# Optimization experiments

Measured on AMD Instinct MI355X. Metric: run time of the kernel, lower is better.

## Reference

```python
import jax, jax.numpy as jnp
import numpy as np

N_NODES = 32
N_HEADS = 4
HEAD_DIM = 64
NEG_SLOPE = 0.2  # PyG GATConv default LeakyReLU slope


def setup_inputs() -> dict:
    key = jax.random.key(0)
    ks = jax.random.split(key, 8)
    roi_feats = jax.random.normal(ks[0], (N_NODES, 256, 96, 96), dtype=jnp.float32)
    edge_index = jax.random.randint(ks[1], (2, 512), 0, N_NODES, dtype=jnp.int32)
    W = jax.random.normal(ks[2], (256, N_HEADS * HEAD_DIM), dtype=jnp.float32) * 0.0625
    a_src = jax.random.normal(ks[3], (N_HEADS, HEAD_DIM), dtype=jnp.float32) * 0.125
    a_dst = jax.random.normal(ks[4], (N_HEADS, HEAD_DIM), dtype=jnp.float32) * 0.125
    gat_bias = jnp.zeros((N_HEADS * HEAD_DIM,), dtype=jnp.float32)
    cls_W = jax.random.normal(ks[5], (256, 32), dtype=jnp.float32) * 0.0625
    cls_b = jnp.zeros((32,), dtype=jnp.float32)
    return {"roi_feats": roi_feats, "edge_index": edge_index, "W": W,
            "a_src": a_src, "a_dst": a_dst, "gat_bias": gat_bias,
            "cls_W": cls_W, "cls_b": cls_b}


def _gat_conv(x, edge_index, W, a_src, a_dst, bias):
    # x: [N, C]; edge_index: [2, E] (src row 0, dst row 1)
    N = x.shape[0]
    # PyG GATConv adds self-loops by default
    loops = jnp.arange(N, dtype=edge_index.dtype)
    src = jnp.concatenate([edge_index[0], loops])
    dst = jnp.concatenate([edge_index[1], loops])
    h = (x @ W).reshape(N, N_HEADS, HEAD_DIM)          # [N, H, F]
    alpha_s = jnp.einsum('nhf,hf->nh', h, a_src)       # [N, H]
    alpha_d = jnp.einsum('nhf,hf->nh', h, a_dst)
    e = alpha_s[src] + alpha_d[dst]                    # [E', H]
    e = jnp.where(e >= 0, e, NEG_SLOPE * e)            # LeakyReLU
    # segment softmax over incoming edges of each dst node
    m = jax.ops.segment_max(e, dst, num_segments=N)    # [N, H]
    ex = jnp.exp(e - m[dst])
    denom = jax.ops.segment_sum(ex, dst, num_segments=N)
    alpha = ex / denom[dst]                            # [E', H]
    out = jax.ops.segment_sum(alpha[:, :, None] * h[src], dst, num_segments=N)
    return out.reshape(N, N_HEADS * HEAD_DIM) + bias


def reference(roi_feats, edge_index, W, a_src, a_dst, gat_bias, cls_W, cls_b):
    # [N, C, H, W] -> [N, C] spatial mean pool
    x = roi_feats.mean(axis=(2, 3))
    x = _gat_conv(x, edge_index, W, a_src, a_dst, gat_bias)
    logit = jax.nn.silu(x) @ cls_W + cls_b             # [N, num_au]
    return logit
```

## Files before the change

### kernel.cpp

```cpp
#include <hip/hip_runtime.h>
#include <math.h>

#define N_NODES  32
#define N_HEADS  4
#define HEAD_DIM 64
#define CDIM     256
#define HWPIX    9216
#define ROWF4    2304
#define E_BASE   512
#define E_TOT    544
#define NEG_SLOPE 0.2f
#define XS       257
#define POOL_BLOCKS 2048

__global__ __launch_bounds__(256, 4) void pool_kernel(const float* __restrict__ roi,
                                                      const float* __restrict__ W,
                                                      const float* __restrict__ a_src,
                                                      const float* __restrict__ a_dst,
                                                      float* __restrict__ x,
                                                      float* __restrict__ was_g,
                                                      float* __restrict__ wad_g) {
    if (blockIdx.x == POOL_BLOCKS) {
        const int t = threadIdx.x;
        float accs[4] = {0.f, 0.f, 0.f, 0.f};
        float accd[4] = {0.f, 0.f, 0.f, 0.f};
        const float4* wr  = (const float4*)(W + (size_t)t * CDIM);
        const float4* as4 = (const float4*)a_src;
        const float4* ad4 = (const float4*)a_dst;
#pragma unroll 16
        for (int j = 0; j < 64; ++j) {
            const float4 w = wr[j], av = as4[j], dv = ad4[j];
            const int hd = j >> 4;
            accs[hd] += w.x * av.x + w.y * av.y + w.z * av.z + w.w * av.w;
            accd[hd] += w.x * dv.x + w.y * dv.y + w.z * dv.z + w.w * dv.w;
        }
#pragma unroll
        for (int hd = 0; hd < 4; ++hd) {
            was_g[t * 4 + hd] = accs[hd];
            wad_g[t * 4 + hd] = accd[hd];
        }
        return;
    }

    const int wave = threadIdx.x >> 6, lane = threadIdx.x & 63;
    const int row = blockIdx.x * 4 + wave;
    const float4* p = reinterpret_cast<const float4*>(roi) + (size_t)row * ROWF4 + lane;

    float4 A[12], B[12];
    float s = 0.f;

#pragma unroll
    for (int j = 0; j < 12; ++j) A[j] = p[j * 64];
#pragma unroll
    for (int j = 0; j < 12; ++j) B[j] = p[(12 + j) * 64];
#pragma unroll
    for (int j = 0; j < 12; ++j) s += (A[j].x + A[j].y) + (A[j].z + A[j].w);
#pragma unroll
    for (int j = 0; j < 12; ++j) A[j] = p[(24 + j) * 64];
#pragma unroll
    for (int j = 0; j < 12; ++j) s += (B[j].x + B[j].y) + (B[j].z + B[j].w);
#pragma unroll
    for (int j = 0; j < 12; ++j) s += (A[j].x + A[j].y) + (A[j].z + A[j].w);

#pragma unroll
    for (int off = 32; off; off >>= 1) s += __shfl_down(s, off);
    if (lane == 0) x[row] = s * (1.0f / (float)HWPIX);
}

__global__ __launch_bounds__(256) void gat_kernel(const int* __restrict__ edge_index,
                                                  const float* __restrict__ x,
                                                  const float* __restrict__ was_g,
                                                  const float* __restrict__ wad_g,
                                                  const float* __restrict__ W,
                                                  const float* __restrict__ gat_bias,
                                                  const float* __restrict__ cls_W,
                                                  const float* __restrict__ cls_b,
                                                  float* __restrict__ out) {
    const int n = blockIdx.x;
    const int t = threadIdx.x;
    const int wavg = t >> 6, lane = t & 63;

    __shared__ float    xs[N_NODES * XS];
    __shared__ float    was[CDIM * N_HEADS];
    __shared__ float    wad[CDIM * N_HEADS];
    __shared__ float    als[N_NODES * N_HEADS];
    __shared__ float    adn[N_HEADS];
    __shared__ unsigned msegu[N_HEADS];
    __shared__ float    M[N_NODES * N_HEADS];
    __shared__ float    y[N_HEADS * CDIM];
    __shared__ float    sv[CDIM];
    __shared__ float4   red4[N_HEADS][64];
    __shared__ float    cred[8][32];

    float4 xv[8];
#pragma unroll
    for (int k = 0; k < 8; ++k) xv[k] = ((const float4*)x)[t + k * 256];
    const float4 wasv = ((const float4*)was_g)[t];
    const float4 wadv = ((const float4*)wad_g)[t];
    const int es0 = edge_index[t],       ed0 = edge_index[E_BASE + t];
    const int es1 = edge_index[256 + t], ed1 = edge_index[E_BASE + 256 + t];
    float4 bias4 = make_float4(0.f, 0.f, 0.f, 0.f);
    if (t < 64) bias4 = ((const float4*)gat_bias)[t];
    float cb = 0.f;
    if (t < 32) cb = cls_b[t];

#pragma unroll
    for (int k = 0; k < 8; ++k) {
        const int i = (t + k * 256) * 4, s = i >> 8, c = i & 255;
        xs[s * XS + c + 0] = xv[k].x;
        xs[s * XS + c + 1] = xv[k].y;
        xs[s * XS + c + 2] = xv[k].z;
        xs[s * XS + c + 3] = xv[k].w;
    }
    ((float4*)was)[t] = wasv;
    ((float4*)wad)[t] = wadv;
    if (t < 128) M[t] = 0.f;
    if (t < 4) msegu[t] = 0u;
    __syncthreads();

    if (t < 132) {
        if (t < 128) {
            const int s = t >> 2, hd = t & 3;
            const float* xrow = &xs[s * XS];
            float acc = 0.f;
#pragma unroll 8
            for (int c = 0; c < CDIM; ++c) acc += xrow[c] * was[c * 4 + hd];
            als[t] = acc;
        } else {
            const int hd = t - 128;
            const float* xrow = &xs[n * XS];
            float acc = 0.f;
#pragma unroll 8
            for (int c = 0; c < CDIM; ++c) acc += xrow[c] * wad[c * 4 + hd];
            adn[hd] = acc;
        }
    }
    __syncthreads();

    {
        const bool sl = (t < 32) && (t == n);
#pragma unroll
        for (int hd = 0; hd < 4; ++hd) {
            float best = -INFINITY;
            if (ed0 == n) {
                float v = als[es0 * 4 + hd] + adn[hd];
                best = fmaxf(best, (v >= 0.f) ? v : NEG_SLOPE * v);
            }
            if (ed1 == n) {
                float v = als[es1 * 4 + hd] + adn[hd];
                best = fmaxf(best, (v >= 0.f) ? v : NEG_SLOPE * v);
            }
            if (sl) {
                float v = als[n * 4 + hd] + adn[hd];
                best = fmaxf(best, (v >= 0.f) ? v : NEG_SLOPE * v);
            }
            if (best > -INFINITY) {
                const int iv = __float_as_int(best);
                const unsigned key = (iv < 0) ? ~(unsigned)iv
                                              : ((unsigned)iv | 0x80000000u);
                atomicMax(&msegu[hd], key);
            }
        }
    }
    __syncthreads();

    float mx[4];
#pragma unroll
    for (int hd = 0; hd < 4; ++hd) {
        const unsigned key = msegu[hd];
        const int im = (key & 0x80000000u) ? (int)(key & 0x7fffffffu) : (int)~key;
        mx[hd] = __int_as_float(im);
    }

    {
        const bool sl = (t < 32) && (t == n);
#pragma unroll
        for (int hd = 0; hd < 4; ++hd) {
            if (ed0 == n) {
                float v = als[es0 * 4 + hd] + adn[hd];
                v = (v >= 0.f) ? v : NEG_SLOPE * v;
                atomicAdd(&M[es0 * 4 + hd], expf(v - mx[hd]));
            }
            if (ed1 == n) {
                float v = als[es1 * 4 + hd] + adn[hd];
                v = (v >= 0.f) ? v : NEG_SLOPE * v;
                atomicAdd(&M[es1 * 4 + hd], expf(v - mx[hd]));
            }
            if (sl) {
                float v = als[n * 4 + hd] + adn[hd];
                v = (v >= 0.f) ? v : NEG_SLOPE * v;
                atomicAdd(&M[n * 4 + hd], expf(v - mx[hd]));
            }
        }
    }
    __syncthreads();

    {
        const int hd = wavg;
        float a0 = 0.f, a1 = 0.f, a2 = 0.f, a3 = 0.f, msum = 0.f;
#pragma unroll
        for (int s = 0; s < N_NODES; ++s) {
            const float m = M[s * 4 + hd];
            msum += m;
            const float* xrow = &xs[s * XS + lane];
            a0 += m * xrow[0];   a1 += m * xrow[64];
            a2 += m * xrow[128]; a3 += m * xrow[192];
        }
        const float rd = 1.0f / msum;
        y[hd * CDIM + lane]       = a0 * rd;
        y[hd * CDIM + lane + 64]  = a1 * rd;
        y[hd * CDIM + lane + 128] = a2 * rd;
        y[hd * CDIM + lane + 192] = a3 * rd;
    }
    __syncthreads();

    {
        const int hd = lane >> 4;
        const float* yrow = &y[hd * CDIM];
        float4 acc = make_float4(0.f, 0.f, 0.f, 0.f);
#pragma unroll 16
        for (int cc = 0; cc < 64; ++cc) {
            const int c = wavg * 64 + cc;
            const float4 w4 = ((const float4*)(W + (size_t)c * CDIM))[lane];
            const float yv = yrow[c];
            acc.x += yv * w4.x; acc.y += yv * w4.y;
            acc.z += yv * w4.z; acc.w += yv * w4.w;
        }
        red4[wavg][lane] = acc;
    }
    __syncthreads();
    if (t < 64) {
        const float4 s0 = red4[0][t], s1 = red4[1][t];
        const float4 s2 = red4[2][t], s3 = red4[3][t];
        float v0 = s0.x + s1.x + s2.x + s3.x + bias4.x;
        float v1 = s0.y + s1.y + s2.y + s3.y + bias4.y;
        float v2 = s0.z + s1.z + s2.z + s3.z + bias4.z;
        float v3 = s0.w + s1.w + s2.w + s3.w + bias4.w;
        sv[4 * t + 0] = v0 / (1.0f + expf(-v0));
        sv[4 * t + 1] = v1 / (1.0f + expf(-v1));
        sv[4 * t + 2] = v2 / (1.0f + expf(-v2));
        sv[4 * t + 3] = v3 / (1.0f + expf(-v3));
    }
    __syncthreads();

    {
        const int j = t & 31, g8 = t >> 5;
        float a = 0.f;
#pragma unroll
        for (int c0 = 0; c0 < 32; ++c0) {
            const int c = g8 * 32 + c0;
            a += sv[c] * cls_W[c * 32 + j];
        }
        cred[g8][j] = a;
    }
    __syncthreads();
    if (t < 32) {
        float s2 = cb;
#pragma unroll
        for (int g2 = 0; g2 < 8; ++g2) s2 += cred[g2][t];
        out[n * 32 + t] = s2;
    }
}

extern "C" void kernel_launch(void* const* d_in, const int* in_sizes, int n_in,
                              void* d_out, int out_size, void* d_ws, size_t ws_size,
                              hipStream_t stream) {
    const float* roi   = (const float*)d_in[0];
    const int*   eidx  = (const int*)d_in[1];
    const float* W     = (const float*)d_in[2];
    const float* a_src = (const float*)d_in[3];
    const float* a_dst = (const float*)d_in[4];
    const float* gbias = (const float*)d_in[5];
    const float* clsW  = (const float*)d_in[6];
    const float* clsb  = (const float*)d_in[7];
    float* out = (float*)d_out;

    float* x     = (float*)d_ws;
    float* was_g = x + 8192;
    float* wad_g = was_g + 1024;

    pool_kernel<<<POOL_BLOCKS + 1, 256, 0, stream>>>(roi, W, a_src, a_dst,
                                                     x, was_g, wad_g);
    gat_kernel<<<N_NODES, 256, 0, stream>>>(eidx, x, was_g, wad_g, W,
                                            gbias, clsW, clsb, out);
}
```

Measured before the change: 64.45 us.

## Widen GAT kernel to 1024 threads and preload W/cls_W into registers

Raises the per-node gat_kernel block from 256 to 1024 threads and redistributes every stage over them. The attention-logit dot products are split four ways with a shuffle reduction, and there is one thread per edge including self-loops. Slices of W and cls_W are prefetched into registers early so their global latency overlaps the softmax stages, and shared scratch buffers are aliased onto the xs region. The aim is to shorten the latency-bound serial chain in this tiny 32-block kernel. The cost is more register pressure and wider cross-wave reductions. The pool kernel, which likely dominates total time, is unchanged.

```diff
diff --git a/kernel.cpp b/kernel.cpp
--- a/kernel.cpp
+++ b/kernel.cpp
@@ -3,7 +3,6 @@
 
 #define N_NODES  32
 #define N_HEADS  4
-#define HEAD_DIM 64
 #define CDIM     256
 #define HWPIX    9216
 #define ROWF4    2304
@@ -67,20 +66,23 @@
     if (lane == 0) x[row] = s * (1.0f / (float)HWPIX);
 }
 
-__global__ __launch_bounds__(256) void gat_kernel(const int* __restrict__ edge_index,
-                                                  const float* __restrict__ x,
-                                                  const float* __restrict__ was_g,
-                                                  const float* __restrict__ wad_g,
-                                                  const float* __restrict__ W,
-                                                  const float* __restrict__ gat_bias,
-                                                  const float* __restrict__ cls_W,
-                                                  const float* __restrict__ cls_b,
-                                                  float* __restrict__ out) {
+__global__ __launch_bounds__(1024, 4) void gat_kernel(const int* __restrict__ edge_index,
+                                                      const float* __restrict__ x,
+                                                      const float* __restrict__ was_g,
+                                                      const float* __restrict__ wad_g,
+                                                      const float* __restrict__ W,
+                                                      const float* __restrict__ gat_bias,
+                                                      const float* __restrict__ cls_W,
+                                                      const float* __restrict__ cls_b,
+                                                      float* __restrict__ out) {
     const int n = blockIdx.x;
     const int t = threadIdx.x;
-    const int wavg = t >> 6, lane = t & 63;
-
-    __shared__ float    xs[N_NODES * XS];
+    const int wv = t >> 6, ln = t & 63;
+
+    __shared__ __align__(16) char arena[N_NODES * XS * 4];
+    float*  xs   = (float*)arena;
+    float4* red4 = (float4*)arena;
+    float*  cred = (float*)(arena + 16384);
     __shared__ float    was[CDIM * N_HEADS];
     __shared__ float    wad[CDIM * N_HEADS];
     __shared__ float    als[N_NODES * N_HEADS];
@@ -89,73 +91,67 @@
     __shared__ float    M[N_NODES * N_HEADS];
     __shared__ float    y[N_HEADS * CDIM];
     __shared__ float    sv[CDIM];
-    __shared__ float4   red4[N_HEADS][64];
-    __shared__ float    cred[8][32];
-
-    float4 xv[8];
-#pragma unroll
-    for (int k = 0; k < 8; ++k) xv[k] = ((const float4*)x)[t + k * 256];
-    const float4 wasv = ((const float4*)was_g)[t];
-    const float4 wadv = ((const float4*)wad_g)[t];
-    const int es0 = edge_index[t],       ed0 = edge_index[E_BASE + t];
-    const int es1 = edge_index[256 + t], ed1 = edge_index[E_BASE + 256 + t];
-    float4 bias4 = make_float4(0.f, 0.f, 0.f, 0.f);
+
+    const float4 xv0 = ((const float4*)x)[t];
+    const float4 xv1 = ((const float4*)x)[t + 1024];
+    float4 wasv = make_float4(0.f,0.f,0.f,0.f), wadv = wasv;
+    if (t < 256) {
+        wasv = ((const float4*)was_g)[t];
+        wadv = ((const float4*)wad_g)[t];
+    }
+    int es0 = 0, ed0 = -1;
+    if (t < E_BASE) { es0 = edge_index[t]; ed0 = edge_index[E_BASE + t]; }
+    float4 bias4 = make_float4(0.f,0.f,0.f,0.f);
     if (t < 64) bias4 = ((const float4*)gat_bias)[t];
     float cb = 0.f;
     if (t < 32) cb = cls_b[t];
-
-#pragma unroll
-    for (int k = 0; k < 8; ++k) {
-        const int i = (t + k * 256) * 4, s = i >> 8, c = i & 255;
-        xs[s * XS + c + 0] = xv[k].x;
-        xs[s * XS + c + 1] = xv[k].y;
-        xs[s * XS + c + 2] = xv[k].z;
-        xs[s * XS + c + 3] = xv[k].w;
-    }
-    ((float4*)was)[t] = wasv;
-    ((float4*)wad)[t] = wadv;
+    float cw[8];
+    {
+        const int k = t & 31, g = t >> 5;
+#pragma unroll
+        for (int i = 0; i < 8; ++i) cw[i] = cls_W[(g * 8 + i) * 32 + k];
+    }
+
+    {
+        int i = t * 4, s = i >> 8, c = i & 255;
+        xs[s * XS + c + 0] = xv0.x; xs[s * XS + c + 1] = xv0.y;
+        xs[s * XS + c + 2] = xv0.z; xs[s * XS + c + 3] = xv0.w;
+        i = (t + 1024) * 4; s = i >> 8; c = i & 255;
+        xs[s * XS + c + 0] = xv1.x; xs[s * XS + c + 1] = xv1.y;
+        xs[s * XS + c + 2] = xv1.z; xs[s * XS + c + 3] = xv1.w;
+    }
+    if (t < 256) { ((float4*)was)[t] = wasv; ((float4*)wad)[t] = wadv; }
     if (t < 128) M[t] = 0.f;
-    if (t < 4) msegu[t] = 0u;
-    __syncthreads();
-
-    if (t < 132) {
-        if (t < 128) {
-            const int s = t >> 2, hd = t & 3;
-            const float* xrow = &xs[s * XS];
-            float acc = 0.f;
-#pragma unroll 8
-            for (int c = 0; c < CDIM; ++c) acc += xrow[c] * was[c * 4 + hd];
-            als[t] = acc;
-        } else {
-            const int hd = t - 128;
-            const float* xrow = &xs[n * XS];
-            float acc = 0.f;
-#pragma unroll 8
-            for (int c = 0; c < CDIM; ++c) acc += xrow[c] * wad[c * 4 + hd];
-            adn[hd] = acc;
-        }
-    }
-    __syncthreads();
-
-    {
-        const bool sl = (t < 32) && (t == n);
-#pragma unroll
-        for (int hd = 0; hd < 4; ++hd) {
-            float best = -INFINITY;
-            if (ed0 == n) {
-                float v = als[es0 * 4 + hd] + adn[hd];
-                best = fmaxf(best, (v >= 0.f) ? v : NEG_SLOPE * v);
-            }
-            if (ed1 == n) {
-                float v = als[es1 * 4 + hd] + adn[hd];
-                best = fmaxf(best, (v >= 0.f) ? v : NEG_SLOPE * v);
-            }
-            if (sl) {
-                float v = als[n * 4 + hd] + adn[hd];
-                best = fmaxf(best, (v >= 0.f) ? v : NEG_SLOPE * v);
-            }
-            if (best > -INFINITY) {
-                const int iv = __float_as_int(best);
+    if (t < 4)   msegu[t] = 0u;
+    __syncthreads();
+
+    if (t < 528) {
+        const int q = t & 3;
+        const int s  = (t < 512) ? (t >> 4) : n;
+        const int hd = (t < 512) ? ((t >> 2) & 3) : ((t - 512) >> 2);
+        const float* xrow = &xs[s * XS + q * 64];
+        const float* wvp  = (t < 512) ? &was[q * 256 + hd] : &wad[q * 256 + hd];
+        float acc = 0.f;
+#pragma unroll 16
+        for (int c = 0; c < 64; ++c) acc += xrow[c] * wvp[c * 4];
+        acc += __shfl_down(acc, 2);
+        acc += __shfl_down(acc, 1);
+        if (q == 0) {
+            if (t < 512) als[(t >> 4) * 4 + hd] = acc;
+            else         adn[hd] = acc;
+        }
+    }
+    __syncthreads();
+
+    if (t < E_TOT) {
+        const int s0 = (t < E_BASE) ? es0 : (t - E_BASE);
+        const int d  = (t < E_BASE) ? ed0 : (t - E_BASE);
+        if (d == n) {
+#pragma unroll
+            for (int hd = 0; hd < 4; ++hd) {
+                float v = als[s0 * 4 + hd] + adn[hd];
+                v = (v >= 0.f) ? v : NEG_SLOPE * v;
+                const int iv = __float_as_int(v);
                 const unsigned key = (iv < 0) ? ~(unsigned)iv
                                               : ((unsigned)iv | 0x80000000u);
                 atomicMax(&msegu[hd], key);
@@ -172,92 +168,76 @@
         mx[hd] = __int_as_float(im);
     }
 
-    {
-        const bool sl = (t < 32) && (t == n);
-#pragma unroll
-        for (int hd = 0; hd < 4; ++hd) {
-            if (ed0 == n) {
-                float v = als[es0 * 4 + hd] + adn[hd];
+    if (t < E_TOT) {
+        const int s0 = (t < E_BASE) ? es0 : (t - E_BASE);
+        const int d  = (t < E_BASE) ? ed0 : (t - E_BASE);
+        if (d == n) {
+#pragma unroll
+            for (int hd = 0; hd < 4; ++hd) {
+                float v = als[s0 * 4 + hd] + adn[hd];
                 v = (v >= 0.f) ? v : NEG_SLOPE * v;
-                atomicAdd(&M[es0 * 4 + hd], expf(v - mx[hd]));
+                atomicAdd(&M[s0 * 4 + hd], expf(v - mx[hd]));
             }
-            if (ed1 == n) {
-                float v = als[es1 * 4 + hd] + adn[hd];
-                v = (v >= 0.f) ? v : NEG_SLOPE * v;
-                atomicAdd(&M[es1 * 4 + hd], expf(v - mx[hd]));
-            }
-            if (sl) {
-                float v = als[n * 4 + hd] + adn[hd];
-                v = (v >= 0.f) ? v : NEG_SLOPE * v;
-                atomicAdd(&M[n * 4 + hd], expf(v - mx[hd]));
-            }
-        }
-    }
-    __syncthreads();
-
-    {
-        const int hd = wavg;
-        float a0 = 0.f, a1 = 0.f, a2 = 0.f, a3 = 0.f, msum = 0.f;
+        }
+    }
+    __syncthreads();
+
+    float4 wreg[16];
+#pragma unroll
+    for (int r = 0; r < 16; ++r)
+        wreg[r] = ((const float4*)(W + (size_t)(wv * 16 + r) * CDIM))[ln];
+
+    {
+        const int hd = t >> 8, c = t & 255;
+        float acc = 0.f, msum = 0.f;
 #pragma unroll
         for (int s = 0; s < N_NODES; ++s) {
             const float m = M[s * 4 + hd];
             msum += m;
-            const float* xrow = &xs[s * XS + lane];
-            a0 += m * xrow[0];   a1 += m * xrow[64];
-            a2 += m * xrow[128]; a3 += m * xrow[192];
-        }
-        const float rd = 1.0f / msum;
-        y[hd * CDIM + lane]       = a0 * rd;
-        y[hd * CDIM + lane + 64]  = a1 * rd;
-        y[hd * CDIM + lane + 128] = a2 * rd;
-        y[hd * CDIM + lane + 192] = a3 * rd;
-    }
-    __syncthreads();
-
-    {
-        const int hd = lane >> 4;
-        const float* yrow = &y[hd * CDIM];
+            acc += m * xs[s * XS + c];
+        }
+        y[hd * CDIM + c] = acc / msum;
+    }
+    __syncthreads();
+
+    {
+        const int hd = ln >> 4;
         float4 acc = make_float4(0.f, 0.f, 0.f, 0.f);
-#pragma unroll 16
-        for (int cc = 0; cc < 64; ++cc) {
-            const int c = wavg * 64 + cc;
-            const float4 w4 = ((const float4*)(W + (size_t)c * CDIM))[lane];
-            const float yv = yrow[c];
-            acc.x += yv * w4.x; acc.y += yv * w4.y;
-            acc.z += yv * w4.z; acc.w += yv * w4.w;
-        }
-        red4[wavg][lane] = acc;
+#pragma unroll
+        for (int r = 0; r < 16; ++r) {
+            const float yv = y[hd * CDIM + wv * 16 + r];
+            acc.x += yv * wreg[r].x; acc.y += yv * wreg[r].y;
+            acc.z += yv * wreg[r].z; acc.w += yv * wreg[r].w;
+        }
+        red4[wv * 64 + ln] = acc;
     }
     __syncthreads();
     if (t < 64) {
-        const float4 s0 = red4[0][t], s1 = red4[1][t];
-        const float4 s2 = red4[2][t], s3 = red4[3][t];
-        float v0 = s0.x + s1.x + s2.x + s3.x + bias4.x;
-        float v1 = s0.y + s1.y + s2.y + s3.y + bias4.y;
-        float v2 = s0.z + s1.z + s2.z + s3.z + bias4.z;
-        float v3 = s0.w + s1.w + s2.w + s3.w + bias4.w;
-        sv[4 * t + 0] = v0 / (1.0f + expf(-v0));
-        sv[4 * t + 1] = v1 / (1.0f + expf(-v1));
-        sv[4 * t + 2] = v2 / (1.0f + expf(-v2));
-        sv[4 * t + 3] = v3 / (1.0f + expf(-v3));
-    }
-    __syncthreads();
-
-    {
-        const int j = t & 31, g8 = t >> 5;
+        float4 a = bias4;
+#pragma unroll
+        for (int g = 0; g < 16; ++g) {
+            const float4 r = red4[g * 64 + t];
+            a.x += r.x; a.y += r.y; a.z += r.z; a.w += r.w;
+        }
+        sv[4 * t + 0] = a.x / (1.0f + expf(-a.x));
+        sv[4 * t + 1] = a.y / (1.0f + expf(-a.y));
+        sv[4 * t + 2] = a.z / (1.0f + expf(-a.z));
+        sv[4 * t + 3] = a.w / (1.0f + expf(-a.w));
+    }
+    __syncthreads();
+
+    {
+        const int k = t & 31, g = t >> 5;
         float a = 0.f;
 #pragma unroll
-        for (int c0 = 0; c0 < 32; ++c0) {
-            const int c = g8 * 32 + c0;
-            a += sv[c] * cls_W[c * 32 + j];
-        }
-        cred[g8][j] = a;
+        for (int i = 0; i < 8; ++i) a += sv[g * 8 + i] * cw[i];
+        cred[g * 32 + k] = a;
     }
     __syncthreads();
     if (t < 32) {
         float s2 = cb;
 #pragma unroll
-        for (int g2 = 0; g2 < 8; ++g2) s2 += cred[g2][t];
+        for (int g = 0; g < 32; ++g) s2 += cred[g * 32 + t];
         out[n * 32 + t] = s2;
     }
 }
@@ -281,6 +261,6 @@
 
     pool_kernel<<<POOL_BLOCKS + 1, 256, 0, stream>>>(roi, W, a_src, a_dst,
                                                      x, was_g, wad_g);
-    gat_kernel<<<N_NODES, 256, 0, stream>>>(eidx, x, was_g, wad_g, W,
-                                            gbias, clsW, clsb, out);
+    gat_kernel<<<N_NODES, 1024, 0, stream>>>(eidx, x, was_g, wad_g, W,
+                                             gbias, clsW, clsb, out);
 }
```

Measured after the change: 63.53 us. No clear change (-1.4%).
